# Kernel tuning notes

Hardware: AMD Instinct MI355X
Metric: run time of the kernel (lower is better)

The kernel has to match this reference:

```python
import jax, jax.numpy as jnp
import numpy as np

D_MODEL = 1024
NUM_HEADS = 16
D_K = D_MODEL // NUM_HEADS


def setup_inputs() -> dict:
    key = jax.random.key(0)
    ks = jax.random.split(key, 11)
    B, S = 4, 2048
    s = 1.0 / np.sqrt(D_MODEL)
    inp = {
        'q': jax.random.normal(ks[0], (B, S, D_MODEL), dtype=jnp.float32),
        'k': jax.random.normal(ks[1], (B, S, D_MODEL), dtype=jnp.float32),
        'v': jax.random.normal(ks[2], (B, S, D_MODEL), dtype=jnp.float32),
        'Wq': jax.random.normal(ks[3], (D_MODEL, D_MODEL), dtype=jnp.float32) * s,
        'bq': jnp.zeros((D_MODEL,), dtype=jnp.float32),
        'Wk': jax.random.normal(ks[4], (D_MODEL, D_MODEL), dtype=jnp.float32) * s,
        'bk': jnp.zeros((D_MODEL,), dtype=jnp.float32),
        'Wv': jax.random.normal(ks[5], (D_MODEL, D_MODEL), dtype=jnp.float32) * s,
        'bv': jnp.zeros((D_MODEL,), dtype=jnp.float32),
        'Wo': jax.random.normal(ks[6], (D_MODEL, D_MODEL), dtype=jnp.float32) * s,
        'bo': jnp.zeros((D_MODEL,), dtype=jnp.float32),
    }
    return inp


def _split_heads(x):
    B, S, _ = x.shape
    return x.reshape(B, S, NUM_HEADS, D_K).transpose(0, 2, 1, 3)  # [B,H,S,d_k]


def reference(q, k, v, Wq, bq, Wk, bk, Wv, bv, Wo, bo):
    B, S, _ = q.shape
    qh = _split_heads(q @ Wq.T + bq)
    kh = _split_heads(k @ Wk.T + bk)
    vh = _split_heads(v @ Wv.T + bv)
    scale = 1.0 / jnp.sqrt(jnp.asarray(D_K, dtype=qh.dtype))
    scores = jnp.einsum('bhqd,bhkd->bhqk', qh, kh) * scale  # [B,H,S,S]
    attn = jax.nn.softmax(scores, axis=-1)
    out = jnp.einsum('bhqk,bhkd->bhqd', attn, vh)  # [B,H,S,d_k]
    out = out.transpose(0, 2, 1, 3).reshape(B, S, D_MODEL)
    return out @ Wo.T + bo
```

## Files before the change

kernel.cpp:

```cpp
#include <hip/hip_runtime.h>


typedef __bf16 bf16_t;
typedef bf16_t bf16x8 __attribute__((ext_vector_type(8)));
typedef bf16_t bf16x4 __attribute__((ext_vector_type(4)));
typedef float  f32x4  __attribute__((ext_vector_type(4)));
typedef short  s16x4  __attribute__((ext_vector_type(4)));

#define MFMA16(A, B, C) __builtin_amdgcn_mfma_f32_16x16x32_bf16(A, B, C, 0, 0, 0)

static __device__ __forceinline__ f32x4 mfma16k16(bf16x4 a, bf16x4 b, f32x4 c) {
  return __builtin_amdgcn_mfma_f32_16x16x16bf16_1k(
      __builtin_bit_cast(s16x4, a), __builtin_bit_cast(s16x4, b), c, 0, 0, 0);
}

#define NB   4
#define SEQ  2048
#define DM   1024
#define NH   16
#define DK   64
#define MTOT (NB * SEQ)
#define QSCALE 0.18033688011112042f

__device__ __forceinline__ void async_copy16(bf16_t* lds, const bf16_t* gsrc) {
  __builtin_amdgcn_global_load_lds(
      (const __attribute__((address_space(1))) unsigned int*)gsrc,
      (__attribute__((address_space(3))) unsigned int*)lds, 16, 0, 0);
}

__device__ __forceinline__ float fast_exp2(float x) {
#if __has_builtin(__builtin_amdgcn_exp2f)
  return __builtin_amdgcn_exp2f(x);
#else
  return exp2f(x);
#endif
}

__global__ __launch_bounds__(256) void cvt3(const float* __restrict__ a,
                                            const float* __restrict__ b,
                                            const float* __restrict__ c,
                                            bf16_t* __restrict__ oa,
                                            bf16_t* __restrict__ ob,
                                            bf16_t* __restrict__ oc, int n4) {
  const int z = blockIdx.y;
  const float* s = (z == 0) ? a : (z == 1) ? b : c;
  bf16_t* d = (z == 0) ? oa : (z == 1) ? ob : oc;
  int i = blockIdx.x * 256 + threadIdx.x;
  if (i < n4) {
    f32x4 v = ((const f32x4*)s)[i];
    ((bf16x4*)d)[i] = __builtin_convertvector(v, bf16x4);
  }
}

__global__ __launch_bounds__(256) void cvt4(const float* __restrict__ a,
                                            const float* __restrict__ b,
                                            const float* __restrict__ c,
                                            const float* __restrict__ dd,
                                            bf16_t* __restrict__ oa,
                                            bf16_t* __restrict__ ob,
                                            bf16_t* __restrict__ oc,
                                            bf16_t* __restrict__ od, int n4) {
  const int z = blockIdx.y;
  const float* s = (z == 0) ? a : (z == 1) ? b : (z == 2) ? c : dd;
  bf16_t* d = (z == 0) ? oa : (z == 1) ? ob : (z == 2) ? oc : od;
  int i = blockIdx.x * 256 + threadIdx.x;
  if (i < n4) {
    f32x4 v = ((const f32x4*)s)[i];
    ((bf16x4*)d)[i] = __builtin_convertvector(v, bf16x4);
  }
}

__device__ __forceinline__ void gemm_core_1024(const bf16_t* __restrict__ A,
                                               const bf16_t* __restrict__ W,
                                               bf16_t* sA, bf16_t* sB,
                                               f32x4 (&acc)[4][4], int m0, int n0) {
  const int tid = threadIdx.x;
  const int lane = tid & 63, r = lane & 15, qd = lane >> 4;
  const int wave = tid >> 6;
  const int wm = (wave & 1) * 64, wn = (wave >> 1) * 64;
  const int arow = tid >> 2, achk = (tid & 3) * 8;
  const bf16_t* gA = A + (size_t)(m0 + arow) * DM + achk;
  const bf16_t* gB = W + (size_t)(n0 + arow) * DM + achk;
  bf16_t* lA = sA + arow * 32 + achk;
  bf16_t* lB = sB + arow * 32 + achk;

#define GSTAGE(buf, k0)                                                       \
  do {                                                                        \
    async_copy16(lA + (buf) * 4096,           gA + (k0));                     \
    async_copy16(lA + (buf) * 4096 + 64 * 32, gA + (k0) + (size_t)64 * DM);   \
    async_copy16(lB + (buf) * 4096,           gB + (k0));                     \
    async_copy16(lB + (buf) * 4096 + 64 * 32, gB + (k0) + (size_t)64 * DM);   \
  } while (0)

  GSTAGE(0, 0);
#pragma unroll 2
  for (int k0 = 0; k0 < DM; k0 += 32) {
    const int buf = (k0 >> 5) & 1;
    __syncthreads();
    if (k0 + 32 < DM) GSTAGE(buf ^ 1, k0 + 32);

    const bf16_t* cA = sA + buf * 4096;
    const bf16_t* cB = sB + buf * 4096;
    bf16x8 af[4], bw[4];
#pragma unroll
    for (int i = 0; i < 4; i++)
      af[i] = *(const bf16x8*)(cA + (wm + i * 16 + r) * 32 + qd * 8);
#pragma unroll
    for (int j = 0; j < 4; j++)
      bw[j] = *(const bf16x8*)(cB + (wn + j * 16 + r) * 32 + qd * 8);
#pragma unroll
    for (int i = 0; i < 4; i++)
#pragma unroll
      for (int j = 0; j < 4; j++)
        acc[i][j] = MFMA16(af[i], bw[j], acc[i][j]);
  }
#undef GSTAGE
}

__global__ __launch_bounds__(256)
void gemm_qkv(const bf16_t* __restrict__ qb, const bf16_t* __restrict__ kb,
              const bf16_t* __restrict__ vb, const bf16_t* __restrict__ wq,
              const bf16_t* __restrict__ wk, const bf16_t* __restrict__ wv,
              const float* __restrict__ bq, const float* __restrict__ bk,
              const float* __restrict__ bv, bf16_t* __restrict__ Qh,
              bf16_t* __restrict__ Kh, bf16_t* __restrict__ Vt) {
  __shared__ __align__(16) bf16_t sA[2 * 128 * 32];
  __shared__ __align__(16) bf16_t sB[2 * 128 * 32];
  const int z = blockIdx.z;
  const bf16_t* A = (z == 0) ? qb : (z == 1) ? kb : vb;
  const bf16_t* W = (z == 0) ? wq : (z == 1) ? wk : wv;
  const float* bias = (z == 0) ? bq : (z == 1) ? bk : bv;
  const int m0 = blockIdx.x * 128, n0 = blockIdx.y * 128;

  f32x4 acc[4][4] = {};
  gemm_core_1024(A, W, sA, sB, acc, m0, n0);

  const int tid = threadIdx.x, lane = tid & 63, r = lane & 15, qd = lane >> 4;
  const int wave = tid >> 6, wm = (wave & 1) * 64, wn = (wave >> 1) * 64;
#pragma unroll
  for (int j = 0; j < 4; j++) {
    const int n = n0 + wn + j * 16 + r;
    const float bs = bias[n];
    const int h = n >> 6, d = n & 63;
#pragma unroll
    for (int i = 0; i < 4; i++) {
#pragma unroll
      for (int rr = 0; rr < 4; rr++) {
        const int m = m0 + wm + i * 16 + qd * 4 + rr;
        const int b_ = m >> 11, s_ = m & 2047;
        float v = acc[i][j][rr] + bs;
        if (z == 0) {
          v *= QSCALE;
          Qh[(((size_t)b_ * NH + h) * SEQ + s_) * DK + d] = (bf16_t)v;
        } else if (z == 1) {
          Kh[(((size_t)b_ * NH + h) * SEQ + s_) * DK + d] = (bf16_t)v;
        } else {
          Vt[(((size_t)b_ * NH + h) * DK + d) * SEQ + s_] = (bf16_t)v;
        }
      }
    }
  }
}

__global__ __launch_bounds__(256)
void gemm_out(const bf16_t* __restrict__ A, const bf16_t* __restrict__ W,
              const float* __restrict__ bias, float* __restrict__ C) {
  __shared__ __align__(16) bf16_t sA[2 * 128 * 32];
  __shared__ __align__(16) bf16_t sB[2 * 128 * 32];
  const int m0 = blockIdx.x * 128, n0 = blockIdx.y * 128;
  f32x4 acc[4][4] = {};
  gemm_core_1024(A, W, sA, sB, acc, m0, n0);

  const int tid = threadIdx.x, lane = tid & 63, r = lane & 15, qd = lane >> 4;
  const int wave = tid >> 6, wm = (wave & 1) * 64, wn = (wave >> 1) * 64;
#pragma unroll
  for (int j = 0; j < 4; j++) {
    const int n = n0 + wn + j * 16 + r;
    const float bs = bias[n];
#pragma unroll
    for (int i = 0; i < 4; i++) {
#pragma unroll
      for (int rr = 0; rr < 4; rr++) {
        const int m = m0 + wm + i * 16 + qd * 4 + rr;
        C[(size_t)m * DM + n] = acc[i][j][rr] + bs;
      }
    }
  }
}

__global__ __launch_bounds__(256)
void attn(const bf16_t* __restrict__ Qh, const bf16_t* __restrict__ Kh,
          const bf16_t* __restrict__ Vt, bf16_t* __restrict__ Ah) {
  __shared__ __align__(16) bf16_t sK[2][128 * 64];
  __shared__ __align__(16) bf16_t sV[2][64 * 128];

  const int tid = threadIdx.x, wave = tid >> 6, lane = tid & 63;
  const int r = lane & 15, qd = lane >> 4;
  const int bh = blockIdx.y;
  const int q0 = blockIdx.x * 128 + wave * 32;
  const size_t bK = (size_t)bh * SEQ * DK;
  const size_t bV = (size_t)bh * DK * SEQ;

  bf16x8 aq[2][2];
#pragma unroll
  for (int qt = 0; qt < 2; qt++)
#pragma unroll
    for (int hf = 0; hf < 2; hf++)
      aq[qt][hf] = *(const bf16x8*)(Qh + bK + (size_t)(q0 + qt * 16 + r) * DK +
                                    hf * 32 + qd * 8);

  f32x4 o[4][2] = {};
  float lsum[2] = {0.f, 0.f};

  const int krow = tid >> 3, kc = tid & 7;
  const int vrow = tid >> 4, vc = tid & 15;

  const bf16_t* gK = Kh + bK + (size_t)krow * DK + ((kc ^ (krow & 7)) * 8);
  const bf16_t* gV = Vt + bV + (size_t)vrow * SEQ + ((vc ^ (vrow & 15)) * 8);

#define STAGE(buf, kv0)                                                        \
  do {                                                                         \
    _Pragma("unroll") for (int it_ = 0; it_ < 4; it_++)                        \
        async_copy16(&sK[buf][0] + it_ * 2048 + tid * 8,                       \
                     gK + (size_t)(kv0 + it_ * 32) * DK);                      \
    _Pragma("unroll") for (int it_ = 0; it_ < 4; it_++)                        \
        async_copy16(&sV[buf][0] + it_ * 2048 + tid * 8,                       \
                     gV + (size_t)it_ * 16 * SEQ + (kv0));                     \
  } while (0)

  STAGE(0, 0);

  for (int it = 0; it < 16; it++) {
    const int buf = it & 1;
    __syncthreads();
    if (it < 15) STAGE(buf ^ 1, (it + 1) * 128);

    const bf16_t* K0 = &sK[buf][0];
    const bf16_t* V0 = &sV[buf][0];

    f32x4 s[2][8];
#pragma unroll
    for (int mt = 0; mt < 8; mt++) {
      const int row = mt * 16 + r;
      bf16x8 ka0 = *(const bf16x8*)(K0 + row * 64 + ((qd ^ (r & 7)) * 8));
      bf16x8 ka1 = *(const bf16x8*)(K0 + row * 64 + (((4 + qd) ^ (r & 7)) * 8));
#pragma unroll
      for (int qt = 0; qt < 2; qt++) {
        f32x4 t = {0.f, 0.f, 0.f, 0.f};
        t = MFMA16(ka0, aq[qt][0], t);
        t = MFMA16(ka1, aq[qt][1], t);
        s[qt][mt] = t;
      }
    }

    bf16x4 p[2][8];
#pragma unroll
    for (int qt = 0; qt < 2; qt++) {
      float ls = 0.f;
#pragma unroll
      for (int mt = 0; mt < 8; mt++) {
        f32x4 e;
#pragma unroll
        for (int rr = 0; rr < 4; rr++) {
          e[rr] = fast_exp2(s[qt][mt][rr]);
          ls += e[rr];
        }
        p[qt][mt] = __builtin_convertvector(e, bf16x4);
      }
      lsum[qt] += ls;
    }

#pragma unroll
    for (int dt = 0; dt < 4; dt++) {
      const int d = dt * 16 + r;
#pragma unroll
      for (int mt = 0; mt < 8; mt++) {
        const int cc = (mt * 2 + (qd >> 1)) ^ r;
        bf16x4 va = *(const bf16x4*)(V0 + d * 128 + cc * 8 + (qd & 1) * 4);
#pragma unroll
        for (int qt = 0; qt < 2; qt++)
          o[dt][qt] = mfma16k16(va, p[qt][mt], o[dt][qt]);
      }
    }
  }

  float linv[2];
#pragma unroll
  for (int qt = 0; qt < 2; qt++) {
    float l = lsum[qt];
    l += __shfl_xor(l, 16);
    l += __shfl_xor(l, 32);
    linv[qt] = 1.0f / l;
  }
  const int b_ = bh >> 4, h_ = bh & 15;
#pragma unroll
  for (int qt = 0; qt < 2; qt++) {
    const size_t rowbase = ((size_t)b_ * SEQ + q0 + qt * 16 + r) * DM + h_ * DK;
#pragma unroll
    for (int dt = 0; dt < 4; dt++) {
      f32x4 w = o[dt][qt] * linv[qt];
      *(bf16x4*)(Ah + rowbase + dt * 16 + qd * 4) =
          __builtin_convertvector(w, bf16x4);
    }
  }
}

extern "C" void kernel_launch(void* const* d_in, const int* in_sizes, int n_in,
                              void* d_out, int out_size, void* d_ws,
                              size_t ws_size, hipStream_t stream) {
  const float* q  = (const float*)d_in[0];
  const float* k  = (const float*)d_in[1];
  const float* v  = (const float*)d_in[2];
  const float* Wq = (const float*)d_in[3];
  const float* bq = (const float*)d_in[4];
  const float* Wk = (const float*)d_in[5];
  const float* bk = (const float*)d_in[6];
  const float* Wv = (const float*)d_in[7];
  const float* bv = (const float*)d_in[8];
  const float* Wo = (const float*)d_in[9];
  const float* bo = (const float*)d_in[10];

  char* ws = (char*)d_ws;
  const size_t SZ_QKV = (size_t)MTOT * DM * 2;
  const size_t SZ_W   = (size_t)DM * DM * 2;
  bf16_t* qb  = (bf16_t*)(ws);
  bf16_t* kb_ = (bf16_t*)(ws + SZ_QKV);
  bf16_t* vb  = (bf16_t*)(ws + 2 * SZ_QKV);
  bf16_t* Wqb = (bf16_t*)(ws + 3 * SZ_QKV);
  bf16_t* Wkb = (bf16_t*)(ws + 3 * SZ_QKV + SZ_W);
  bf16_t* Wvb = (bf16_t*)(ws + 3 * SZ_QKV + 2 * SZ_W);
  bf16_t* Wob = (bf16_t*)(ws + 3 * SZ_QKV + 3 * SZ_W);
  bf16_t* Qh  = (bf16_t*)(ws + 3 * SZ_QKV + 4 * SZ_W);
  bf16_t* Kh  = (bf16_t*)(ws + 4 * SZ_QKV + 4 * SZ_W);
  bf16_t* Vt  = (bf16_t*)(ws + 5 * SZ_QKV + 4 * SZ_W);
  bf16_t* Ah  = (bf16_t*)(ws + 6 * SZ_QKV + 4 * SZ_W);

  const int n4_qkv = MTOT * DM / 4;
  const int n4_w   = DM * DM / 4;
  cvt3<<<dim3(n4_qkv / 256, 3), 256, 0, stream>>>(q, k, v, qb, kb_, vb, n4_qkv);
  cvt4<<<dim3(n4_w / 256, 4), 256, 0, stream>>>(Wq, Wk, Wv, Wo, Wqb, Wkb, Wvb,
                                                Wob, n4_w);

  gemm_qkv<<<dim3(64, 8, 3), 256, 0, stream>>>(qb, kb_, vb, Wqb, Wkb, Wvb, bq,
                                               bk, bv, Qh, Kh, Vt);

  attn<<<dim3(16, 64), 256, 0, stream>>>(Qh, Kh, Vt, Ah);

  gemm_out<<<dim3(64, 8), 256, 0, stream>>>(Ah, Wob, bo, (float*)d_out);
}
```

Before: 379.2 us.

## Remap attention blocks per XCD, MFMA row sums, re-swizzle V layout

Attention launches as a 1D grid and remaps block ids so that all query tiles of one batch-head land on the same XCD, aiming to improve L2 reuse of K and V. The softmax row sum is now computed with an MFMA against a ones vector instead of scalar adds and cross-lane shuffles, moving that work from VALU to the matrix unit. The V transpose store and the LDS read use a new 4-element XOR swizzle so the attention kernel can read V with simpler indexing and fewer bank conflicts. Summing the bf16-rounded probabilities changes numerics slightly, and the layout change couples the QKV GEMM epilogue to the attention reader.

```diff
diff --git a/kernel.cpp b/kernel.cpp
--- a/kernel.cpp
+++ b/kernel.cpp
@@ -155,7 +155,8 @@
         } else if (z == 1) {
           Kh[(((size_t)b_ * NH + h) * SEQ + s_) * DK + d] = (bf16_t)v;
         } else {
-          Vt[(((size_t)b_ * NH + h) * DK + d) * SEQ + s_] = (bf16_t)v;
+          Vt[(((size_t)b_ * NH + h) * DK + d) * SEQ + (s_ ^ ((d & 1) * 4))] =
+              (bf16_t)v;
         }
       }
     }
@@ -196,8 +197,10 @@
 
   const int tid = threadIdx.x, wave = tid >> 6, lane = tid & 63;
   const int r = lane & 15, qd = lane >> 4;
-  const int bh = blockIdx.y;
-  const int q0 = blockIdx.x * 128 + wave * 32;
+  const int id = blockIdx.x;
+  const int xcd = id & 7, sub = id >> 3;
+  const int bh = xcd * 8 + (sub >> 4);
+  const int q0 = (sub & 15) * 128 + wave * 32;
   const size_t bK = (size_t)bh * SEQ * DK;
   const size_t bV = (size_t)bh * DK * SEQ;
 
@@ -210,13 +213,16 @@
                                     hf * 32 + qd * 8);
 
   f32x4 o[4][2] = {};
-  float lsum[2] = {0.f, 0.f};
+  f32x4 lacc[2] = {};
+  bf16x4 vone;
+#pragma unroll
+  for (int i = 0; i < 4; i++) vone[i] = (bf16_t)1.0f;
 
   const int krow = tid >> 3, kc = tid & 7;
   const int vrow = tid >> 4, vc = tid & 15;
 
   const bf16_t* gK = Kh + bK + (size_t)krow * DK + ((kc ^ (krow & 7)) * 8);
-  const bf16_t* gV = Vt + bV + (size_t)vrow * SEQ + ((vc ^ (vrow & 15)) * 8);
+  const bf16_t* gV = Vt + bV + (size_t)vrow * SEQ + ((vc ^ ((vrow >> 1) & 7)) * 8);
 
 #define STAGE(buf, kv0)                                                        \
   do {                                                                         \
@@ -256,18 +262,14 @@
     bf16x4 p[2][8];
 #pragma unroll
     for (int qt = 0; qt < 2; qt++) {
-      float ls = 0.f;
 #pragma unroll
       for (int mt = 0; mt < 8; mt++) {
         f32x4 e;
 #pragma unroll
-        for (int rr = 0; rr < 4; rr++) {
-          e[rr] = fast_exp2(s[qt][mt][rr]);
-          ls += e[rr];
-        }
+        for (int rr = 0; rr < 4; rr++) e[rr] = fast_exp2(s[qt][mt][rr]);
         p[qt][mt] = __builtin_convertvector(e, bf16x4);
-      }
-      lsum[qt] += ls;
+        lacc[qt] = mfma16k16(vone, p[qt][mt], lacc[qt]);
+      }
     }
 
 #pragma unroll
@@ -275,8 +277,7 @@
       const int d = dt * 16 + r;
 #pragma unroll
       for (int mt = 0; mt < 8; mt++) {
-        const int cc = (mt * 2 + (qd >> 1)) ^ r;
-        bf16x4 va = *(const bf16x4*)(V0 + d * 128 + cc * 8 + (qd & 1) * 4);
+        bf16x4 va = *(const bf16x4*)(V0 + d * 128 + (((mt * 4 + qd) ^ r) * 4));
 #pragma unroll
         for (int qt = 0; qt < 2; qt++)
           o[dt][qt] = mfma16k16(va, p[qt][mt], o[dt][qt]);
@@ -284,21 +285,16 @@
     }
   }
 
-  float linv[2];
+  const float linv0 = 1.0f / lacc[0][0];
+  const float linv1 = 1.0f / lacc[1][0];
+  const int b_ = bh >> 4, h_ = bh & 15;
 #pragma unroll
   for (int qt = 0; qt < 2; qt++) {
-    float l = lsum[qt];
-    l += __shfl_xor(l, 16);
-    l += __shfl_xor(l, 32);
-    linv[qt] = 1.0f / l;
-  }
-  const int b_ = bh >> 4, h_ = bh & 15;
-#pragma unroll
-  for (int qt = 0; qt < 2; qt++) {
+    const float linv = qt ? linv1 : linv0;
     const size_t rowbase = ((size_t)b_ * SEQ + q0 + qt * 16 + r) * DM + h_ * DK;
 #pragma unroll
     for (int dt = 0; dt < 4; dt++) {
-      f32x4 w = o[dt][qt] * linv[qt];
+      f32x4 w = o[dt][qt] * linv;
       *(bf16x4*)(Ah + rowbase + dt * 16 + qd * 4) =
           __builtin_convertvector(w, bf16x4);
     }
@@ -344,7 +340,7 @@
   gemm_qkv<<<dim3(64, 8, 3), 256, 0, stream>>>(qb, kb_, vb, Wqb, Wkb, Wvb, bq,
                                                bk, bv, Qh, Kh, Vt);
 
-  attn<<<dim3(16, 64), 256, 0, stream>>>(Qh, Kh, Vt, Ah);
+  attn<<<dim3(1024), 256, 0, stream>>>(Qh, Kh, Vt, Ah);
 
   gemm_out<<<dim3(64, 8), 256, 0, stream>>>(Ah, Wob, bo, (float*)d_out);
 }
```

New measurement: 378.4 us. No clear change (-0.2%).
